# Kernel optimization log

Hardware: AMD Instinct MI355X
Metric: run time of the kernel (lower is better)

Reference implementation:

```python
import jax, jax.numpy as jnp
import numpy as np

EPS = 1e-5

def _segment_mean(src_feat, edge_index, num_targets):
    # src_feat: [Ns, D]; edge_index: [2, E] = [source_idx, target_idx]
    msgs = src_feat[edge_index[0]]                                   # [E, D] gather
    agg = jax.ops.segment_sum(msgs, edge_index[1], num_segments=num_targets)
    deg = jax.ops.segment_sum(jnp.ones((edge_index.shape[1],), src_feat.dtype),
                              edge_index[1], num_segments=num_targets)
    return agg / jnp.clip(deg, 1.0)[:, None]

def _layernorm(x, gamma, beta):
    mu = jnp.mean(x, axis=-1, keepdims=True)
    var = jnp.mean(jnp.square(x - mu), axis=-1, keepdims=True)
    return (x - mu) * jax.lax.rsqrt(var + EPS) * gamma + beta

def setup_inputs() -> dict:
    key = jax.random.key(0)
    ks = jax.random.split(key, 8)
    NU, NI, E, D = 50000, 50000, 300000, 256
    s = 1.0 / np.sqrt(D)
    return {
        "user_features": jax.random.normal(ks[0], (NU, D), jnp.float32),
        "item_features": jax.random.normal(ks[1], (NI, D), jnp.float32),
        "user_item_edge_index": jax.random.randint(ks[2], (2, E), 0, NI),
        "item_user_edge_index": jax.random.randint(ks[3], (2, E), 0, NU),
        "Wu": jax.random.uniform(ks[4], (D, D), jnp.float32, -s, s),
        "bu": jax.random.uniform(ks[5], (D,), jnp.float32, -s, s),
        "Wi": jax.random.uniform(ks[6], (D, D), jnp.float32, -s, s),
        "bi": jax.random.uniform(ks[7], (D,), jnp.float32, -s, s),
        "gamma": jnp.ones((D,), jnp.float32),
        "beta": jnp.zeros((D,), jnp.float32),
    }

def reference(user_features, item_features, user_item_edge_index, item_user_edge_index,
              Wu, bu, Wi, bi, gamma, beta):
    num_items = item_features.shape[0]
    num_users = user_features.shape[0]
    # messages into items come from users; into users come from items
    item_messages = _segment_mean(user_features, user_item_edge_index, num_items)
    user_messages = _segment_mean(item_features, item_user_edge_index, num_users)
    u_new = (user_features + user_messages) @ Wu + bu
    i_new = (item_features + item_messages) @ Wi + bi
    u_new = _layernorm(jax.nn.relu(u_new), gamma, beta)
    i_new = _layernorm(jax.nn.relu(i_new), gamma, beta)
    return (u_new, i_new)
```

## Files before the change

### kernel.cpp

```cpp
#include <hip/hip_runtime.h>
#include <hip/hip_bf16.h>

#define D 256
#define BM 64
#define BM2 32
#define LDA 264
#define LDK 72

typedef __attribute__((ext_vector_type(8))) __bf16 bf16x8;
typedef __attribute__((ext_vector_type(4))) float f32x4;

__device__ __forceinline__ float bf2f(unsigned short u) {
    union { unsigned int i; float f; } c; c.i = ((unsigned int)u) << 16; return c.f;
}
__device__ __forceinline__ float bf2f_lo(unsigned int u) {
    union { unsigned int i; float f; } c; c.i = u << 16; return c.f;
}
__device__ __forceinline__ float bf2f_hi(unsigned int u) {
    union { unsigned int i; float f; } c; c.i = u & 0xffff0000u; return c.f;
}
__device__ __forceinline__ unsigned short f2bf(float f) {
    __hip_bfloat16 h = __float2bfloat16(f);
    return *reinterpret_cast<unsigned short*>(&h);
}
__device__ __forceinline__ unsigned int pack2(float lo, float hi) {
    return (unsigned int)f2bf(lo) | ((unsigned int)f2bf(hi) << 16);
}


__global__ void k_prep(const float* __restrict__ uf, const float* __restrict__ itf,
                       const float* __restrict__ Wu, const float* __restrict__ Wi,
                       unsigned short* __restrict__ feat_bf,
                       unsigned short* __restrict__ Wt_u, unsigned short* __restrict__ Wt_i,
                       const int* __restrict__ iu_e, int Eiu,
                       const int* __restrict__ ui_e, int Eui,
                       int* __restrict__ deg, int NU,
                       size_t nfU, size_t nfTot, int nbF) {
    int b = blockIdx.x;
    if (b < nbF) {
        size_t base = ((size_t)b * 256 + threadIdx.x) * 8;
        if (base < nfTot) {
            const float* s = (base < nfU) ? (uf + base) : (itf + (base - nfU));
            float4 f0 = *(const float4*)s;
            float4 f1 = *(const float4*)(s + 4);
            ushort4 o0, o1;
            o0.x = f2bf(f0.x); o0.y = f2bf(f0.y); o0.z = f2bf(f0.z); o0.w = f2bf(f0.w);
            o1.x = f2bf(f1.x); o1.y = f2bf(f1.y); o1.z = f2bf(f1.z); o1.w = f2bf(f1.w);
            ((ushort4*)(feat_bf + base))[0] = o0;
            ((ushort4*)(feat_bf + base))[1] = o1;
        }
    } else if (b < nbF + 512) {
        int b2 = b - nbF;
        const float* W = (b2 < 256) ? Wu : Wi;
        unsigned short* Wt = (b2 < 256) ? Wt_u : Wt_i;
        int k = b2 & 255;
        int c = threadIdx.x;
        Wt[(size_t)c * 256 + k] = f2bf(W[(size_t)k * 256 + c]);
    } else {
        int e = (b - nbF - 512) * 256 + threadIdx.x;
        if (e < Eiu) {
            atomicAdd(&deg[iu_e[Eiu + e]], 1);
        } else if (e < Eiu + Eui) {
            int e2 = e - Eiu;
            atomicAdd(&deg[NU + ui_e[Eui + e2]], 1);
        }
    }
}

__global__ void k_scan_block(const int* __restrict__ deg, int N,
                             int* __restrict__ rs, int* __restrict__ bsums) {
    __shared__ int s[1024];
    int base = blockIdx.x * 1024;
    int t = threadIdx.x;
    int v = (base + t < N) ? deg[base + t] : 0;
    s[t] = v;
    __syncthreads();
    for (int off = 1; off < 1024; off <<= 1) {
        int add = (t >= off) ? s[t - off] : 0;
        __syncthreads();
        s[t] += add;
        __syncthreads();
    }
    if (base + t < N) rs[base + t + 1] = s[t];
    if (t == 1023) bsums[blockIdx.x] = s[1023];
}

__global__ void k_scan_sums(int* __restrict__ bsums, int nb) {
    __shared__ int s[1024];
    int t = threadIdx.x;
    int v = (t < nb) ? bsums[t] : 0;
    s[t] = v;
    __syncthreads();
    for (int off = 1; off < 1024; off <<= 1) {
        int add = (t >= off) ? s[t - off] : 0;
        __syncthreads();
        s[t] += add;
        __syncthreads();
    }
    if (t < nb) bsums[t] = s[t] - v;
}

__global__ void k_finalize(int N, int* __restrict__ rs, int* __restrict__ cur,
                           const int* __restrict__ bsums) {
    int i = blockIdx.x * blockDim.x + threadIdx.x;
    if (i < N) {
        int v = rs[i + 1] + bsums[i >> 10];
        rs[i + 1] = v;
        cur[i + 1] = v;
    }
    if (i == 0) { rs[0] = 0; cur[0] = 0; }
}

__global__ void k_fill2(const int* __restrict__ iu_e, int Eiu,
                        const int* __restrict__ ui_e, int Eui,
                        int* __restrict__ cur, int NU,
                        int* __restrict__ csr) {
    int e = blockIdx.x * blockDim.x + threadIdx.x;
    if (e < Eiu) {
        int d = iu_e[Eiu + e];
        int p = atomicAdd(&cur[d], 1);
        csr[p] = iu_e[e];
    } else if (e < Eiu + Eui) {
        int e2 = e - Eiu;
        int d = ui_e[Eui + e2];
        int p = atomicAdd(&cur[NU + d], 1);
        csr[p] = ui_e[e2];
    }
}

__global__ void k_msg2(const unsigned short* __restrict__ uf_bf,
                       const unsigned short* __restrict__ if_bf,
                       const int* __restrict__ rs, const int* __restrict__ csr,
                       unsigned short* __restrict__ x_u, unsigned short* __restrict__ x_i,
                       int NU, int NI) {
    int pair = (blockIdx.x * blockDim.x + threadIdx.x) >> 6;
    int lane = threadIdx.x & 63;
    int half = lane >> 5;
    int hl   = lane & 31;
    int Ntot = NU + NI;
    int wv = pair * 2 + half;
    if (wv >= Ntot) return;

    const unsigned short* src; const unsigned short* tgt; unsigned short* xo; int w;
    if (wv < NU) { src = if_bf; tgt = uf_bf; xo = x_u; w = wv; }
    else         { src = uf_bf; tgt = if_bf; xo = x_i; w = wv - NU; }

    int s0 = rs[wv], s1 = rs[wv + 1];
    float a0[8] = {}, a1[8] = {}, a2[8] = {}, a3[8] = {};

    int i = s0;
    for (; i + 4 <= s1; i += 4) {
        int e0 = csr[i], e1 = csr[i + 1], e2 = csr[i + 2], e3 = csr[i + 3];
        uint4 r0 = ((const uint4*)(src + (size_t)e0 * D))[hl];
        uint4 r1 = ((const uint4*)(src + (size_t)e1 * D))[hl];
        uint4 r2 = ((const uint4*)(src + (size_t)e2 * D))[hl];
        uint4 r3 = ((const uint4*)(src + (size_t)e3 * D))[hl];
        a0[0] += bf2f_lo(r0.x); a0[1] += bf2f_hi(r0.x); a0[2] += bf2f_lo(r0.y); a0[3] += bf2f_hi(r0.y);
        a0[4] += bf2f_lo(r0.z); a0[5] += bf2f_hi(r0.z); a0[6] += bf2f_lo(r0.w); a0[7] += bf2f_hi(r0.w);
        a1[0] += bf2f_lo(r1.x); a1[1] += bf2f_hi(r1.x); a1[2] += bf2f_lo(r1.y); a1[3] += bf2f_hi(r1.y);
        a1[4] += bf2f_lo(r1.z); a1[5] += bf2f_hi(r1.z); a1[6] += bf2f_lo(r1.w); a1[7] += bf2f_hi(r1.w);
        a2[0] += bf2f_lo(r2.x); a2[1] += bf2f_hi(r2.x); a2[2] += bf2f_lo(r2.y); a2[3] += bf2f_hi(r2.y);
        a2[4] += bf2f_lo(r2.z); a2[5] += bf2f_hi(r2.z); a2[6] += bf2f_lo(r2.w); a2[7] += bf2f_hi(r2.w);
        a3[0] += bf2f_lo(r3.x); a3[1] += bf2f_hi(r3.x); a3[2] += bf2f_lo(r3.y); a3[3] += bf2f_hi(r3.y);
        a3[4] += bf2f_lo(r3.z); a3[5] += bf2f_hi(r3.z); a3[6] += bf2f_lo(r3.w); a3[7] += bf2f_hi(r3.w);
    }
    for (; i < s1; ++i) {
        int e0 = csr[i];
        uint4 r0 = ((const uint4*)(src + (size_t)e0 * D))[hl];
        a0[0] += bf2f_lo(r0.x); a0[1] += bf2f_hi(r0.x); a0[2] += bf2f_lo(r0.y); a0[3] += bf2f_hi(r0.y);
        a0[4] += bf2f_lo(r0.z); a0[5] += bf2f_hi(r0.z); a0[6] += bf2f_lo(r0.w); a0[7] += bf2f_hi(r0.w);
    }

    int cnt = s1 - s0;
    float inv = 1.0f / (float)(cnt > 0 ? cnt : 1);
    uint4 tv = ((const uint4*)(tgt + (size_t)w * D))[hl];
    float x0 = bf2f_lo(tv.x) + (a0[0] + a1[0] + a2[0] + a3[0]) * inv;
    float x1 = bf2f_hi(tv.x) + (a0[1] + a1[1] + a2[1] + a3[1]) * inv;
    float x2 = bf2f_lo(tv.y) + (a0[2] + a1[2] + a2[2] + a3[2]) * inv;
    float x3 = bf2f_hi(tv.y) + (a0[3] + a1[3] + a2[3] + a3[3]) * inv;
    float x4 = bf2f_lo(tv.z) + (a0[4] + a1[4] + a2[4] + a3[4]) * inv;
    float x5 = bf2f_hi(tv.z) + (a0[5] + a1[5] + a2[5] + a3[5]) * inv;
    float x6 = bf2f_lo(tv.w) + (a0[6] + a1[6] + a2[6] + a3[6]) * inv;
    float x7 = bf2f_hi(tv.w) + (a0[7] + a1[7] + a2[7] + a3[7]) * inv;
    uint4 o;
    o.x = pack2(x0, x1); o.y = pack2(x2, x3); o.z = pack2(x4, x5); o.w = pack2(x6, x7);
    ((uint4*)(xo + (size_t)w * D))[hl] = o;
}

__launch_bounds__(256)
__global__ void k_gemm5(const unsigned short* __restrict__ x_u,
                        const unsigned short* __restrict__ x_i,
                        const unsigned short* __restrict__ Wt_u,
                        const unsigned short* __restrict__ Wt_i,
                        const float* __restrict__ bu, const float* __restrict__ bi,
                        const float* __restrict__ gamma, const float* __restrict__ beta,
                        int NU, int NI, int nbU, float* __restrict__ out) {
    __shared__ __align__(16) __hip_bfloat16 As[BM2][LDA];
    __shared__ float red_s[BM2][4];
    __shared__ float red_q[BM2][4];

    int b = blockIdx.x;
    bool isU = b < nbU;
    const unsigned short* X  = isU ? x_u : x_i;
    const unsigned short* Wt = isU ? Wt_u : Wt_i;
    const float* bias        = isU ? bu : bi;
    float* Y                 = isU ? out : out + (size_t)NU * D;
    int N                    = isU ? NU : NI;
    int row0 = (isU ? b : b - nbU) * BM2;

    int t = threadIdx.x;
    int lane = t & 63;
    int w = t >> 6;
    int l15 = lane & 15;
    int l4 = lane >> 4;

    {
        const uint4* Xg = (const uint4*)&X[(size_t)row0 * D];
        #pragma unroll
        for (int j = 0; j < 4; ++j) {
            int f = j * 256 + t;
            int lr = f >> 5;
            int c = f & 31;
            uint4 v = {0, 0, 0, 0};
            if (row0 + lr < N) v = Xg[(size_t)lr * 32 + c];
            *(uint4*)&As[lr][c * 8] = v;
        }
    }

    f32x4 acc[2][4];
    f32x4 zero = {0.f, 0.f, 0.f, 0.f};
    #pragma unroll
    for (int fr = 0; fr < 2; fr++)
        #pragma unroll
        for (int fc = 0; fc < 4; fc++)
            acc[fr][fc] = zero;

    __syncthreads();

    const uint4* Bg = (const uint4*)Wt;
    int colB = w * 64 + l15;
    #pragma unroll
    for (int ks8 = 0; ks8 < 8; ++ks8) {
        uint4 bq[4];
        #pragma unroll
        for (int fc = 0; fc < 4; ++fc)
            bq[fc] = Bg[(size_t)(colB + fc * 16) * 32 + ks8 * 4 + l4];
        bf16x8 af[2];
        #pragma unroll
        for (int fr = 0; fr < 2; ++fr)
            af[fr] = *(const bf16x8*)&As[fr * 16 + l15][ks8 * 32 + l4 * 8];
        #pragma unroll
        for (int fr = 0; fr < 2; ++fr)
            #pragma unroll
            for (int fc = 0; fc < 4; ++fc)
                acc[fr][fc] = __builtin_amdgcn_mfma_f32_16x16x32_bf16(
                    af[fr], *(bf16x8*)&bq[fc], acc[fr][fc], 0, 0, 0);
    }

    float bias_c[4], gam_c[4], bet_c[4];
    #pragma unroll
    for (int fc = 0; fc < 4; fc++) {
        int col = w * 64 + fc * 16 + l15;
        bias_c[fc] = bias[col];
        gam_c[fc]  = gamma[col];
        bet_c[fc]  = beta[col];
    }

    #pragma unroll
    for (int fr = 0; fr < 2; fr++) {
        #pragma unroll
        for (int r = 0; r < 4; r++) {
            int row = fr * 16 + l4 * 4 + r;
            float s = 0.f, q = 0.f;
            #pragma unroll
            for (int fc = 0; fc < 4; fc++) {
                float v = acc[fr][fc][r] + bias_c[fc];
                v = fmaxf(v, 0.f);
                acc[fr][fc][r] = v;
                s += v;
                q += v * v;
            }
            #pragma unroll
            for (int m = 1; m < 16; m <<= 1) {
                s += __shfl_xor(s, m);
                q += __shfl_xor(q, m);
            }
            if (l15 == 0) { red_s[row][w] = s; red_q[row][w] = q; }
        }
    }
    __syncthreads();

    #pragma unroll
    for (int fr = 0; fr < 2; fr++) {
        #pragma unroll
        for (int r = 0; r < 4; r++) {
            int row = fr * 16 + l4 * 4 + r;
            int grow = row0 + row;
            if (grow >= N) continue;
            float s = red_s[row][0] + red_s[row][1] + red_s[row][2] + red_s[row][3];
            float q = red_q[row][0] + red_q[row][1] + red_q[row][2] + red_q[row][3];
            float mu  = s * (1.0f / 256.0f);
            float var = q * (1.0f / 256.0f) - mu * mu;
            float rstd = rsqrtf(var + 1e-5f);
            #pragma unroll
            for (int fc = 0; fc < 4; fc++) {
                int col = w * 64 + fc * 16 + l15;
                Y[(size_t)grow * D + col] = (acc[fr][fc][r] - mu) * rstd * gam_c[fc] + bet_c[fc];
            }
        }
    }
}


__global__ void k_hist(const int* __restrict__ dst, int E, int* __restrict__ deg) {
    int e = blockIdx.x * blockDim.x + threadIdx.x;
    if (e < E) atomicAdd(&deg[dst[e]], 1);
}

__global__ void k_finalize_rs(int N, int* __restrict__ rs, const int* __restrict__ bsums) {
    int i = blockIdx.x * blockDim.x + threadIdx.x;
    if (i < N) rs[i + 1] += bsums[i >> 10];
    if (i == 0) rs[0] = 0;
}

__global__ void k_fill(const int* __restrict__ src, const int* __restrict__ dst, int E,
                       const int* __restrict__ rs, int* __restrict__ cursor,
                       int* __restrict__ csr) {
    int e = blockIdx.x * blockDim.x + threadIdx.x;
    if (e < E) {
        int d = dst[e];
        int p = atomicAdd(&cursor[d], 1);
        csr[rs[d] + p] = src[e];
    }
}

__global__ void k_msg_x(const float* __restrict__ srcf, const float* __restrict__ tgtf,
                        const int* __restrict__ rs, const int* __restrict__ csr,
                        int N, float* __restrict__ xout) {
    int wave = (blockIdx.x * blockDim.x + threadIdx.x) >> 6;
    int lane = threadIdx.x & 63;
    if (wave >= N) return;
    int s0 = rs[wave], s1 = rs[wave + 1];
    float4 acc = make_float4(0.f, 0.f, 0.f, 0.f);
    for (int i = s0; i < s1; i++) {
        int s = csr[i];
        float4 f = *(const float4*)&srcf[(size_t)s * D + lane * 4];
        acc.x += f.x; acc.y += f.y; acc.z += f.z; acc.w += f.w;
    }
    int cnt = s1 - s0;
    float inv = 1.0f / (float)(cnt > 0 ? cnt : 1);
    float4 t = *(const float4*)&tgtf[(size_t)wave * D + lane * 4];
    float4 x;
    x.x = t.x + acc.x * inv;
    x.y = t.y + acc.y * inv;
    x.z = t.z + acc.z * inv;
    x.w = t.w + acc.w * inv;
    *(float4*)&xout[(size_t)wave * D + lane * 4] = x;
}

__global__ void k_wcvt(const float* __restrict__ W0, const float* __restrict__ W1,
                       __hip_bfloat16* __restrict__ Wt0, __hip_bfloat16* __restrict__ Wt1) {
    int b = blockIdx.x;
    const float* W = (b < 256) ? W0 : W1;
    __hip_bfloat16* Wt = (b < 256) ? Wt0 : Wt1;
    int k = b & 255;
    int c = threadIdx.x;
    Wt[(size_t)c * 256 + k] = __float2bfloat16(W[(size_t)k * 256 + c]);
}

__launch_bounds__(256)
__global__ void k_gemm_mfma_ln(const float* __restrict__ X,
                               const __hip_bfloat16* __restrict__ Wt,
                               const float* __restrict__ bias,
                               const float* __restrict__ gamma,
                               const float* __restrict__ beta,
                               int N, float* __restrict__ Y) {
    __shared__ __hip_bfloat16 As[BM][LDK];
    __shared__ __hip_bfloat16 Bs[D][LDK];
    __shared__ float red_s[BM][4];
    __shared__ float red_q[BM][4];

    int t = threadIdx.x;
    int lane = t & 63;
    int w = t >> 6;
    int l15 = lane & 15;
    int l4 = lane >> 4;
    int row0 = blockIdx.x * BM;

    f32x4 acc[4][4];
    f32x4 zero = {0.f, 0.f, 0.f, 0.f};
    #pragma unroll
    for (int fr = 0; fr < 4; fr++)
        #pragma unroll
        for (int fc = 0; fc < 4; fc++)
            acc[fr][fc] = zero;

    for (int k0 = 0; k0 < D; k0 += 64) {
        {
            int i = t >> 2;
            int kq = (t & 3) * 16;
            int r = row0 + i;
            float4 f[4];
            if (r < N) {
                const float4* p = (const float4*)&X[(size_t)r * D + k0 + kq];
                f[0] = p[0]; f[1] = p[1]; f[2] = p[2]; f[3] = p[3];
            } else {
                float4 z4 = make_float4(0.f, 0.f, 0.f, 0.f);
                f[0] = z4; f[1] = z4; f[2] = z4; f[3] = z4;
            }
            __hip_bfloat16 vb[16];
            #pragma unroll
            for (int q = 0; q < 4; q++) {
                vb[q * 4 + 0] = __float2bfloat16(f[q].x);
                vb[q * 4 + 1] = __float2bfloat16(f[q].y);
                vb[q * 4 + 2] = __float2bfloat16(f[q].z);
                vb[q * 4 + 3] = __float2bfloat16(f[q].w);
            }
            *(uint4*)&As[i][kq]     = *(uint4*)&vb[0];
            *(uint4*)&As[i][kq + 8] = *(uint4*)&vb[8];
        }
        #pragma unroll
        for (int pass = 0; pass < 4; pass++) {
            int c = pass * 64 + (t >> 2);
            int kq = (t & 3) * 16;
            const uint4* p = (const uint4*)&Wt[(size_t)c * D + k0 + kq];
            uint4 b0 = p[0], b1 = p[1];
            *(uint4*)&Bs[c][kq]     = b0;
            *(uint4*)&Bs[c][kq + 8] = b1;
        }
        __syncthreads();

        #pragma unroll
        for (int ks = 0; ks < 2; ks++) {
            bf16x8 af[4], bg[4];
            #pragma unroll
            for (int fr = 0; fr < 4; fr++)
                af[fr] = *(const bf16x8*)&As[fr * 16 + l15][ks * 32 + l4 * 8];
            #pragma unroll
            for (int fc = 0; fc < 4; fc++)
                bg[fc] = *(const bf16x8*)&Bs[w * 64 + fc * 16 + l15][ks * 32 + l4 * 8];
            #pragma unroll
            for (int fr = 0; fr < 4; fr++)
                #pragma unroll
                for (int fc = 0; fc < 4; fc++)
                    acc[fr][fc] = __builtin_amdgcn_mfma_f32_16x16x32_bf16(
                        af[fr], bg[fc], acc[fr][fc], 0, 0, 0);
        }
        __syncthreads();
    }

    float bias_c[4], gam_c[4], bet_c[4];
    #pragma unroll
    for (int fc = 0; fc < 4; fc++) {
        int col = w * 64 + fc * 16 + l15;
        bias_c[fc] = bias[col];
        gam_c[fc]  = gamma[col];
        bet_c[fc]  = beta[col];
    }

    #pragma unroll
    for (int fr = 0; fr < 4; fr++) {
        #pragma unroll
        for (int r = 0; r < 4; r++) {
            int row = fr * 16 + l4 * 4 + r;
            float s = 0.f, q = 0.f;
            #pragma unroll
            for (int fc = 0; fc < 4; fc++) {
                float v = acc[fr][fc][r] + bias_c[fc];
                v = fmaxf(v, 0.f);
                acc[fr][fc][r] = v;
                s += v;
                q += v * v;
            }
            #pragma unroll
            for (int m = 1; m < 16; m <<= 1) {
                s += __shfl_xor(s, m);
                q += __shfl_xor(q, m);
            }
            if (l15 == 0) { red_s[row][w] = s; red_q[row][w] = q; }
        }
    }
    __syncthreads();

    #pragma unroll
    for (int fr = 0; fr < 4; fr++) {
        #pragma unroll
        for (int r = 0; r < 4; r++) {
            int row = fr * 16 + l4 * 4 + r;
            int grow = row0 + row;
            if (grow >= N) continue;
            float s = red_s[row][0] + red_s[row][1] + red_s[row][2] + red_s[row][3];
            float q = red_q[row][0] + red_q[row][1] + red_q[row][2] + red_q[row][3];
            float mu  = s * (1.0f / 256.0f);
            float var = q * (1.0f / 256.0f) - mu * mu;
            float rstd = rsqrtf(var + 1e-5f);
            #pragma unroll
            for (int fc = 0; fc < 4; fc++) {
                int col = w * 64 + fc * 16 + l15;
                Y[(size_t)grow * D + col] = (acc[fr][fc][r] - mu) * rstd * gam_c[fc] + bet_c[fc];
            }
        }
    }
}


extern "C" void kernel_launch(void* const* d_in, const int* in_sizes, int n_in,
                              void* d_out, int out_size, void* d_ws, size_t ws_size,
                              hipStream_t stream) {
    const float* uf    = (const float*)d_in[0];
    const float* itf   = (const float*)d_in[1];
    const int*   ui_e  = (const int*)d_in[2];
    const int*   iu_e  = (const int*)d_in[3];
    const float* Wu    = (const float*)d_in[4];
    const float* bu    = (const float*)d_in[5];
    const float* Wi    = (const float*)d_in[6];
    const float* bi    = (const float*)d_in[7];
    const float* gamma = (const float*)d_in[8];
    const float* beta  = (const float*)d_in[9];

    int NU  = in_sizes[0] / D;
    int NI  = in_sizes[1] / D;
    int Eui = in_sizes[2] / 2;
    int Eiu = in_sizes[3] / 2;
    int Nmax = NU > NI ? NU : NI;
    int Ntot = NU + NI;
    int Etot = Eiu + Eui;

    float* out   = (float*)d_out;
    size_t nfU = (size_t)NU * D;
    size_t nfI = (size_t)NI * D;
    size_t nfTot = nfU + nfI;

    unsigned short* uf_bf = (unsigned short*)d_ws;
    unsigned short* if_bf = uf_bf + nfU;
    unsigned short* x_u   = if_bf + nfI;
    unsigned short* x_i   = x_u + nfU;
    unsigned short* Wt_u2 = x_i + nfI;
    unsigned short* Wt_i2 = Wt_u2 + 65536;
    int* deg2  = (int*)(Wt_i2 + 65536);
    int* rs2   = deg2 + Ntot;
    int* cur2  = rs2 + Ntot + 1;
    int* bsums = cur2 + Ntot + 1;
    int* csr2  = bsums + 1024;
    size_t needed = (size_t)((char*)(csr2 + Etot) - (char*)d_ws);

    if (ws_size >= needed) {
        int nbF = (int)((nfTot + 2047) / 2048);
        int nbH = (Etot + 255) / 256;
        hipMemsetAsync(deg2, 0, (size_t)Ntot * sizeof(int), stream);
        k_prep<<<nbF + 512 + nbH, 256, 0, stream>>>(uf, itf, Wu, Wi, uf_bf, Wt_u2, Wt_i2,
                                                    iu_e, Eiu, ui_e, Eui, deg2, NU,
                                                    nfU, nfTot, nbF);
        int nb = (Ntot + 1023) / 1024;
        k_scan_block<<<nb, 1024, 0, stream>>>(deg2, Ntot, rs2, bsums);
        k_scan_sums<<<1, 1024, 0, stream>>>(bsums, nb);
        k_finalize<<<(Ntot + 255) / 256, 256, 0, stream>>>(Ntot, rs2, cur2, bsums);
        k_fill2<<<nbH, 256, 0, stream>>>(iu_e, Eiu, ui_e, Eui, cur2, NU, csr2);
        int pairs = (Ntot + 1) / 2;
        k_msg2<<<(pairs + 3) / 4, 256, 0, stream>>>(uf_bf, if_bf, rs2, csr2, x_u, x_i, NU, NI);
        int nbU = (NU + BM2 - 1) / BM2;
        int nbI = (NI + BM2 - 1) / BM2;
        k_gemm5<<<nbU + nbI, 256, 0, stream>>>(x_u, x_i, Wt_u2, Wt_i2, bu, bi, gamma, beta,
                                               NU, NI, nbU, out);
        return;
    }

    float* u_out = out;
    float* i_out = out + nfU;
    __hip_bfloat16* Wt_u = (__hip_bfloat16*)d_ws;
    __hip_bfloat16* Wt_i = Wt_u + 256 * 256;
    int* deg    = (int*)(Wt_i + 256 * 256);
    int* rs     = deg + Nmax;
    int* bs     = rs + Nmax + 1;
    int* cursor = bs + 1024;
    int* csr    = cursor + Nmax;

    k_wcvt<<<512, 256, 0, stream>>>(Wu, Wi, Wt_u, Wt_i);

    auto run_side = [&](const float* srcf, const float* tgtf, const int* edges, int E,
                        int N, const __hip_bfloat16* Wt, const float* bias, float* y) {
        const int* esrc = edges;
        const int* edst = edges + E;
        hipMemsetAsync(deg, 0, (size_t)N * sizeof(int), stream);
        hipMemsetAsync(cursor, 0, (size_t)N * sizeof(int), stream);
        k_hist<<<(E + 255) / 256, 256, 0, stream>>>(edst, E, deg);
        int nb = (N + 1023) / 1024;
        k_scan_block<<<nb, 1024, 0, stream>>>(deg, N, rs, bs);
        k_scan_sums<<<1, 1024, 0, stream>>>(bs, nb);
        k_finalize_rs<<<(N + 255) / 256, 256, 0, stream>>>(N, rs, bs);
        k_fill<<<(E + 255) / 256, 256, 0, stream>>>(esrc, edst, E, rs, cursor, csr);
        k_msg_x<<<(N + 3) / 4, 256, 0, stream>>>(srcf, tgtf, rs, csr, N, y);
        k_gemm_mfma_ln<<<(N + BM - 1) / BM, 256, 0, stream>>>(y, Wt, bias, gamma, beta, N, y);
    };

    run_side(itf, uf, iu_e, Eiu, NU, Wt_u, bu, u_out);
    run_side(uf, itf, ui_e, Eui, NI, Wt_i, bi, i_out);
}
```

Before: 218.0 us.

## Overlap item message aggregation with user GEMM in a mixed kernel

```diff
diff --git a/kernel.cpp b/kernel.cpp
--- a/kernel.cpp
+++ b/kernel.cpp
@@ -25,6 +25,163 @@
 }
 __device__ __forceinline__ unsigned int pack2(float lo, float hi) {
     return (unsigned int)f2bf(lo) | ((unsigned int)f2bf(hi) << 16);
+}
+
+
+__device__ __forceinline__ void msg_pair_body(
+    const unsigned short* __restrict__ src, const unsigned short* __restrict__ tgt,
+    const int* __restrict__ rs, const int* __restrict__ csr,
+    unsigned short* __restrict__ xo, int rsBase, int N, int pair, int lane) {
+    int half = lane >> 5;
+    int hl   = lane & 31;
+    int w = pair * 2 + half;
+    if (w >= N) return;
+    int wv = rsBase + w;
+    int s0 = rs[wv], s1 = rs[wv + 1];
+    float a0[8] = {}, a1[8] = {}, a2[8] = {}, a3[8] = {};
+    int i = s0;
+    for (; i + 4 <= s1; i += 4) {
+        int e0 = csr[i], e1 = csr[i + 1], e2 = csr[i + 2], e3 = csr[i + 3];
+        uint4 r0 = ((const uint4*)(src + (size_t)e0 * D))[hl];
+        uint4 r1 = ((const uint4*)(src + (size_t)e1 * D))[hl];
+        uint4 r2 = ((const uint4*)(src + (size_t)e2 * D))[hl];
+        uint4 r3 = ((const uint4*)(src + (size_t)e3 * D))[hl];
+        a0[0] += bf2f_lo(r0.x); a0[1] += bf2f_hi(r0.x); a0[2] += bf2f_lo(r0.y); a0[3] += bf2f_hi(r0.y);
+        a0[4] += bf2f_lo(r0.z); a0[5] += bf2f_hi(r0.z); a0[6] += bf2f_lo(r0.w); a0[7] += bf2f_hi(r0.w);
+        a1[0] += bf2f_lo(r1.x); a1[1] += bf2f_hi(r1.x); a1[2] += bf2f_lo(r1.y); a1[3] += bf2f_hi(r1.y);
+        a1[4] += bf2f_lo(r1.z); a1[5] += bf2f_hi(r1.z); a1[6] += bf2f_lo(r1.w); a1[7] += bf2f_hi(r1.w);
+        a2[0] += bf2f_lo(r2.x); a2[1] += bf2f_hi(r2.x); a2[2] += bf2f_lo(r2.y); a2[3] += bf2f_hi(r2.y);
+        a2[4] += bf2f_lo(r2.z); a2[5] += bf2f_hi(r2.z); a2[6] += bf2f_lo(r2.w); a2[7] += bf2f_hi(r2.w);
+        a3[0] += bf2f_lo(r3.x); a3[1] += bf2f_hi(r3.x); a3[2] += bf2f_lo(r3.y); a3[3] += bf2f_hi(r3.y);
+        a3[4] += bf2f_lo(r3.z); a3[5] += bf2f_hi(r3.z); a3[6] += bf2f_lo(r3.w); a3[7] += bf2f_hi(r3.w);
+    }
+    for (; i < s1; ++i) {
+        int e0 = csr[i];
+        uint4 r0 = ((const uint4*)(src + (size_t)e0 * D))[hl];
+        a0[0] += bf2f_lo(r0.x); a0[1] += bf2f_hi(r0.x); a0[2] += bf2f_lo(r0.y); a0[3] += bf2f_hi(r0.y);
+        a0[4] += bf2f_lo(r0.z); a0[5] += bf2f_hi(r0.z); a0[6] += bf2f_lo(r0.w); a0[7] += bf2f_hi(r0.w);
+    }
+    int cnt = s1 - s0;
+    float inv = 1.0f / (float)(cnt > 0 ? cnt : 1);
+    uint4 tv = ((const uint4*)(tgt + (size_t)w * D))[hl];
+    float x0 = bf2f_lo(tv.x) + (a0[0] + a1[0] + a2[0] + a3[0]) * inv;
+    float x1 = bf2f_hi(tv.x) + (a0[1] + a1[1] + a2[1] + a3[1]) * inv;
+    float x2 = bf2f_lo(tv.y) + (a0[2] + a1[2] + a2[2] + a3[2]) * inv;
+    float x3 = bf2f_hi(tv.y) + (a0[3] + a1[3] + a2[3] + a3[3]) * inv;
+    float x4 = bf2f_lo(tv.z) + (a0[4] + a1[4] + a2[4] + a3[4]) * inv;
+    float x5 = bf2f_hi(tv.z) + (a0[5] + a1[5] + a2[5] + a3[5]) * inv;
+    float x6 = bf2f_lo(tv.w) + (a0[6] + a1[6] + a2[6] + a3[6]) * inv;
+    float x7 = bf2f_hi(tv.w) + (a0[7] + a1[7] + a2[7] + a3[7]) * inv;
+    uint4 o;
+    o.x = pack2(x0, x1); o.y = pack2(x2, x3); o.z = pack2(x4, x5); o.w = pack2(x6, x7);
+    ((uint4*)(xo + (size_t)w * D))[hl] = o;
+}
+
+__device__ __forceinline__ void gemm_tile_body(
+    const unsigned short* __restrict__ X, const unsigned short* __restrict__ Wt,
+    const float* __restrict__ bias, const float* __restrict__ gamma,
+    const float* __restrict__ beta, int N, float* __restrict__ Y, int row0, int t,
+    __hip_bfloat16 (*As)[LDA], float (*red_s)[4], float (*red_q)[4]) {
+    int lane = t & 63;
+    int w = t >> 6;
+    int l15 = lane & 15;
+    int l4 = lane >> 4;
+
+    {
+        const uint4* Xg = (const uint4*)&X[(size_t)row0 * D];
+        #pragma unroll
+        for (int j = 0; j < 4; ++j) {
+            int f = j * 256 + t;
+            int lr = f >> 5;
+            int c = f & 31;
+            uint4 v = {0, 0, 0, 0};
+            if (row0 + lr < N) v = Xg[(size_t)lr * 32 + c];
+            *(uint4*)&As[lr][c * 8] = v;
+        }
+    }
+
+    f32x4 acc[2][4];
+    f32x4 zero = {0.f, 0.f, 0.f, 0.f};
+    #pragma unroll
+    for (int fr = 0; fr < 2; fr++)
+        #pragma unroll
+        for (int fc = 0; fc < 4; fc++)
+            acc[fr][fc] = zero;
+
+    __syncthreads();
+
+    const uint4* Bg = (const uint4*)Wt;
+    int colB = w * 64 + l15;
+    #pragma unroll
+    for (int ks8 = 0; ks8 < 8; ++ks8) {
+        uint4 bq[4];
+        #pragma unroll
+        for (int fc = 0; fc < 4; ++fc)
+            bq[fc] = Bg[(size_t)(colB + fc * 16) * 32 + ks8 * 4 + l4];
+        bf16x8 af[2];
+        #pragma unroll
+        for (int fr = 0; fr < 2; ++fr)
+            af[fr] = *(const bf16x8*)&As[fr * 16 + l15][ks8 * 32 + l4 * 8];
+        #pragma unroll
+        for (int fr = 0; fr < 2; ++fr)
+            #pragma unroll
+            for (int fc = 0; fc < 4; ++fc)
+                acc[fr][fc] = __builtin_amdgcn_mfma_f32_16x16x32_bf16(
+                    af[fr], *(bf16x8*)&bq[fc], acc[fr][fc], 0, 0, 0);
+    }
+
+    float bias_c[4], gam_c[4], bet_c[4];
+    #pragma unroll
+    for (int fc = 0; fc < 4; fc++) {
+        int col = w * 64 + fc * 16 + l15;
+        bias_c[fc] = bias[col];
+        gam_c[fc]  = gamma[col];
+        bet_c[fc]  = beta[col];
+    }
+
+    #pragma unroll
+    for (int fr = 0; fr < 2; fr++) {
+        #pragma unroll
+        for (int r = 0; r < 4; r++) {
+            int row = fr * 16 + l4 * 4 + r;
+            float s = 0.f, q = 0.f;
+            #pragma unroll
+            for (int fc = 0; fc < 4; fc++) {
+                float v = acc[fr][fc][r] + bias_c[fc];
+                v = fmaxf(v, 0.f);
+                acc[fr][fc][r] = v;
+                s += v;
+                q += v * v;
+            }
+            #pragma unroll
+            for (int m = 1; m < 16; m <<= 1) {
+                s += __shfl_xor(s, m);
+                q += __shfl_xor(q, m);
+            }
+            if (l15 == 0) { red_s[row][w] = s; red_q[row][w] = q; }
+        }
+    }
+    __syncthreads();
+
+    #pragma unroll
+    for (int fr = 0; fr < 2; fr++) {
+        #pragma unroll
+        for (int r = 0; r < 4; r++) {
+            int row = fr * 16 + l4 * 4 + r;
+            int grow = row0 + row;
+            if (grow >= N) continue;
+            float s = red_s[row][0] + red_s[row][1] + red_s[row][2] + red_s[row][3];
+            float q = red_q[row][0] + red_q[row][1] + red_q[row][2] + red_q[row][3];
+            float mu  = s * (1.0f / 256.0f);
+            float var = q * (1.0f / 256.0f) - mu * mu;
+            float rstd = rsqrtf(var + 1e-5f);
+            #pragma unroll
+            for (int fc = 0; fc < 4; fc++) {
+                int col = w * 64 + fc * 16 + l15;
+                Y[(size_t)grow * D + col] = (acc[fr][fc][r] - mu) * rstd * gam_c[fc] + bet_c[fc];
+            }
+        }
+    }
 }
 
 
@@ -128,187 +285,48 @@
     }
 }
 
-__global__ void k_msg2(const unsigned short* __restrict__ uf_bf,
+__global__ void k_msgU(const unsigned short* __restrict__ uf_bf,
                        const unsigned short* __restrict__ if_bf,
                        const int* __restrict__ rs, const int* __restrict__ csr,
-                       unsigned short* __restrict__ x_u, unsigned short* __restrict__ x_i,
-                       int NU, int NI) {
+                       unsigned short* __restrict__ x_u, int NU) {
     int pair = (blockIdx.x * blockDim.x + threadIdx.x) >> 6;
-    int lane = threadIdx.x & 63;
-    int half = lane >> 5;
-    int hl   = lane & 31;
-    int Ntot = NU + NI;
-    int wv = pair * 2 + half;
-    if (wv >= Ntot) return;
-
-    const unsigned short* src; const unsigned short* tgt; unsigned short* xo; int w;
-    if (wv < NU) { src = if_bf; tgt = uf_bf; xo = x_u; w = wv; }
-    else         { src = uf_bf; tgt = if_bf; xo = x_i; w = wv - NU; }
-
-    int s0 = rs[wv], s1 = rs[wv + 1];
-    float a0[8] = {}, a1[8] = {}, a2[8] = {}, a3[8] = {};
-
-    int i = s0;
-    for (; i + 4 <= s1; i += 4) {
-        int e0 = csr[i], e1 = csr[i + 1], e2 = csr[i + 2], e3 = csr[i + 3];
-        uint4 r0 = ((const uint4*)(src + (size_t)e0 * D))[hl];
-        uint4 r1 = ((const uint4*)(src + (size_t)e1 * D))[hl];
-        uint4 r2 = ((const uint4*)(src + (size_t)e2 * D))[hl];
-        uint4 r3 = ((const uint4*)(src + (size_t)e3 * D))[hl];
-        a0[0] += bf2f_lo(r0.x); a0[1] += bf2f_hi(r0.x); a0[2] += bf2f_lo(r0.y); a0[3] += bf2f_hi(r0.y);
-        a0[4] += bf2f_lo(r0.z); a0[5] += bf2f_hi(r0.z); a0[6] += bf2f_lo(r0.w); a0[7] += bf2f_hi(r0.w);
-        a1[0] += bf2f_lo(r1.x); a1[1] += bf2f_hi(r1.x); a1[2] += bf2f_lo(r1.y); a1[3] += bf2f_hi(r1.y);
-        a1[4] += bf2f_lo(r1.z); a1[5] += bf2f_hi(r1.z); a1[6] += bf2f_lo(r1.w); a1[7] += bf2f_hi(r1.w);
-        a2[0] += bf2f_lo(r2.x); a2[1] += bf2f_hi(r2.x); a2[2] += bf2f_lo(r2.y); a2[3] += bf2f_hi(r2.y);
-        a2[4] += bf2f_lo(r2.z); a2[5] += bf2f_hi(r2.z); a2[6] += bf2f_lo(r2.w); a2[7] += bf2f_hi(r2.w);
-        a3[0] += bf2f_lo(r3.x); a3[1] += bf2f_hi(r3.x); a3[2] += bf2f_lo(r3.y); a3[3] += bf2f_hi(r3.y);
-        a3[4] += bf2f_lo(r3.z); a3[5] += bf2f_hi(r3.z); a3[6] += bf2f_lo(r3.w); a3[7] += bf2f_hi(r3.w);
-    }
-    for (; i < s1; ++i) {
-        int e0 = csr[i];
-        uint4 r0 = ((const uint4*)(src + (size_t)e0 * D))[hl];
-        a0[0] += bf2f_lo(r0.x); a0[1] += bf2f_hi(r0.x); a0[2] += bf2f_lo(r0.y); a0[3] += bf2f_hi(r0.y);
-        a0[4] += bf2f_lo(r0.z); a0[5] += bf2f_hi(r0.z); a0[6] += bf2f_lo(r0.w); a0[7] += bf2f_hi(r0.w);
-    }
-
-    int cnt = s1 - s0;
-    float inv = 1.0f / (float)(cnt > 0 ? cnt : 1);
-    uint4 tv = ((const uint4*)(tgt + (size_t)w * D))[hl];
-    float x0 = bf2f_lo(tv.x) + (a0[0] + a1[0] + a2[0] + a3[0]) * inv;
-    float x1 = bf2f_hi(tv.x) + (a0[1] + a1[1] + a2[1] + a3[1]) * inv;
-    float x2 = bf2f_lo(tv.y) + (a0[2] + a1[2] + a2[2] + a3[2]) * inv;
-    float x3 = bf2f_hi(tv.y) + (a0[3] + a1[3] + a2[3] + a3[3]) * inv;
-    float x4 = bf2f_lo(tv.z) + (a0[4] + a1[4] + a2[4] + a3[4]) * inv;
-    float x5 = bf2f_hi(tv.z) + (a0[5] + a1[5] + a2[5] + a3[5]) * inv;
-    float x6 = bf2f_lo(tv.w) + (a0[6] + a1[6] + a2[6] + a3[6]) * inv;
-    float x7 = bf2f_hi(tv.w) + (a0[7] + a1[7] + a2[7] + a3[7]) * inv;
-    uint4 o;
-    o.x = pack2(x0, x1); o.y = pack2(x2, x3); o.z = pack2(x4, x5); o.w = pack2(x6, x7);
-    ((uint4*)(xo + (size_t)w * D))[hl] = o;
+    msg_pair_body(if_bf, uf_bf, rs, csr, x_u, 0, NU, pair, threadIdx.x & 63);
 }
 
 __launch_bounds__(256)
-__global__ void k_gemm5(const unsigned short* __restrict__ x_u,
-                        const unsigned short* __restrict__ x_i,
-                        const unsigned short* __restrict__ Wt_u,
-                        const unsigned short* __restrict__ Wt_i,
-                        const float* __restrict__ bu, const float* __restrict__ bi,
-                        const float* __restrict__ gamma, const float* __restrict__ beta,
-                        int NU, int NI, int nbU, float* __restrict__ out) {
+__global__ void k_mix(const unsigned short* __restrict__ uf_bf,
+                      const unsigned short* __restrict__ if_bf,
+                      const int* __restrict__ rs, const int* __restrict__ csr,
+                      unsigned short* __restrict__ x_i,
+                      const unsigned short* __restrict__ x_u,
+                      const unsigned short* __restrict__ Wt_u,
+                      const float* __restrict__ bu,
+                      const float* __restrict__ gamma, const float* __restrict__ beta,
+                      int NU, int NI, int nbMsgI, float* __restrict__ out) {
     __shared__ __align__(16) __hip_bfloat16 As[BM2][LDA];
     __shared__ float red_s[BM2][4];
     __shared__ float red_q[BM2][4];
-
-    int b = blockIdx.x;
-    bool isU = b < nbU;
-    const unsigned short* X  = isU ? x_u : x_i;
-    const unsigned short* Wt = isU ? Wt_u : Wt_i;
-    const float* bias        = isU ? bu : bi;
-    float* Y                 = isU ? out : out + (size_t)NU * D;
-    int N                    = isU ? NU : NI;
-    int row0 = (isU ? b : b - nbU) * BM2;
-
     int t = threadIdx.x;
-    int lane = t & 63;
-    int w = t >> 6;
-    int l15 = lane & 15;
-    int l4 = lane >> 4;
-
-    {
-        const uint4* Xg = (const uint4*)&X[(size_t)row0 * D];
-        #pragma unroll
-        for (int j = 0; j < 4; ++j) {
-            int f = j * 256 + t;
-            int lr = f >> 5;
-            int c = f & 31;
-            uint4 v = {0, 0, 0, 0};
-            if (row0 + lr < N) v = Xg[(size_t)lr * 32 + c];
-            *(uint4*)&As[lr][c * 8] = v;
-        }
-    }
-
-    f32x4 acc[2][4];
-    f32x4 zero = {0.f, 0.f, 0.f, 0.f};
-    #pragma unroll
-    for (int fr = 0; fr < 2; fr++)
-        #pragma unroll
-        for (int fc = 0; fc < 4; fc++)
-            acc[fr][fc] = zero;
-
-    __syncthreads();
-
-    const uint4* Bg = (const uint4*)Wt;
-    int colB = w * 64 + l15;
-    #pragma unroll
-    for (int ks8 = 0; ks8 < 8; ++ks8) {
-        uint4 bq[4];
-        #pragma unroll
-        for (int fc = 0; fc < 4; ++fc)
-            bq[fc] = Bg[(size_t)(colB + fc * 16) * 32 + ks8 * 4 + l4];
-        bf16x8 af[2];
-        #pragma unroll
-        for (int fr = 0; fr < 2; ++fr)
-            af[fr] = *(const bf16x8*)&As[fr * 16 + l15][ks8 * 32 + l4 * 8];
-        #pragma unroll
-        for (int fr = 0; fr < 2; ++fr)
-            #pragma unroll
-            for (int fc = 0; fc < 4; ++fc)
-                acc[fr][fc] = __builtin_amdgcn_mfma_f32_16x16x32_bf16(
-                    af[fr], *(bf16x8*)&bq[fc], acc[fr][fc], 0, 0, 0);
-    }
-
-    float bias_c[4], gam_c[4], bet_c[4];
-    #pragma unroll
-    for (int fc = 0; fc < 4; fc++) {
-        int col = w * 64 + fc * 16 + l15;
-        bias_c[fc] = bias[col];
-        gam_c[fc]  = gamma[col];
-        bet_c[fc]  = beta[col];
-    }
-
-    #pragma unroll
-    for (int fr = 0; fr < 2; fr++) {
-        #pragma unroll
-        for (int r = 0; r < 4; r++) {
-            int row = fr * 16 + l4 * 4 + r;
-            float s = 0.f, q = 0.f;
-            #pragma unroll
-            for (int fc = 0; fc < 4; fc++) {
-                float v = acc[fr][fc][r] + bias_c[fc];
-                v = fmaxf(v, 0.f);
-                acc[fr][fc][r] = v;
-                s += v;
-                q += v * v;
-            }
-            #pragma unroll
-            for (int m = 1; m < 16; m <<= 1) {
-                s += __shfl_xor(s, m);
-                q += __shfl_xor(q, m);
-            }
-            if (l15 == 0) { red_s[row][w] = s; red_q[row][w] = q; }
-        }
-    }
-    __syncthreads();
-
-    #pragma unroll
-    for (int fr = 0; fr < 2; fr++) {
-        #pragma unroll
-        for (int r = 0; r < 4; r++) {
-            int row = fr * 16 + l4 * 4 + r;
-            int grow = row0 + row;
-            if (grow >= N) continue;
-            float s = red_s[row][0] + red_s[row][1] + red_s[row][2] + red_s[row][3];
-            float q = red_q[row][0] + red_q[row][1] + red_q[row][2] + red_q[row][3];
-            float mu  = s * (1.0f / 256.0f);
-            float var = q * (1.0f / 256.0f) - mu * mu;
-            float rstd = rsqrtf(var + 1e-5f);
-            #pragma unroll
-            for (int fc = 0; fc < 4; fc++) {
-                int col = w * 64 + fc * 16 + l15;
-                Y[(size_t)grow * D + col] = (acc[fr][fc][r] - mu) * rstd * gam_c[fc] + bet_c[fc];
-            }
-        }
-    }
+    if (blockIdx.x < nbMsgI) {
+        int pair = (blockIdx.x * 256 + t) >> 6;
+        msg_pair_body(uf_bf, if_bf, rs, csr, x_i, NU, NI, pair, t & 63);
+    } else {
+        int b = blockIdx.x - nbMsgI;
+        gemm_tile_body(x_u, Wt_u, bu, gamma, beta, NU, out, b * BM2, t, As, red_s, red_q);
+    }
+}
+
+__launch_bounds__(256)
+__global__ void k_gemmI(const unsigned short* __restrict__ x_i,
+                        const unsigned short* __restrict__ Wt_i,
+                        const float* __restrict__ bi,
+                        const float* __restrict__ gamma, const float* __restrict__ beta,
+                        int NU, int NI, float* __restrict__ out) {
+    __shared__ __align__(16) __hip_bfloat16 As[BM2][LDA];
+    __shared__ float red_s[BM2][4];
+    __shared__ float red_q[BM2][4];
+    gemm_tile_body(x_i, Wt_i, bi, gamma, beta, NI, out + (size_t)NU * D,
+                   blockIdx.x * BM2, threadIdx.x, As, red_s, red_q);
 }
 
 
@@ -556,12 +574,17 @@
         k_scan_sums<<<1, 1024, 0, stream>>>(bsums, nb);
         k_finalize<<<(Ntot + 255) / 256, 256, 0, stream>>>(Ntot, rs2, cur2, bsums);
         k_fill2<<<nbH, 256, 0, stream>>>(iu_e, Eiu, ui_e, Eui, cur2, NU, csr2);
-        int pairs = (Ntot + 1) / 2;
-        k_msg2<<<(pairs + 3) / 4, 256, 0, stream>>>(uf_bf, if_bf, rs2, csr2, x_u, x_i, NU, NI);
-        int nbU = (NU + BM2 - 1) / BM2;
-        int nbI = (NI + BM2 - 1) / BM2;
-        k_gemm5<<<nbU + nbI, 256, 0, stream>>>(x_u, x_i, Wt_u2, Wt_i2, bu, bi, gamma, beta,
-                                               NU, NI, nbU, out);
+
+        int pairsU = (NU + 1) / 2;
+        k_msgU<<<(pairsU + 3) / 4, 256, 0, stream>>>(uf_bf, if_bf, rs2, csr2, x_u, NU);
+        int pairsI = (NI + 1) / 2;
+        int nbMsgI = (pairsI + 3) / 4;
+        int nbGemmU = (NU + BM2 - 1) / BM2;
+        k_mix<<<nbMsgI + nbGemmU, 256, 0, stream>>>(uf_bf, if_bf, rs2, csr2, x_i, x_u,
+                                                    Wt_u2, bu, gamma, beta,
+                                                    NU, NI, nbMsgI, out);
+        int nbGemmI = (NI + BM2 - 1) / BM2;
+        k_gemmI<<<nbGemmI, 256, 0, stream>>>(x_i, Wt_i2, bi, gamma, beta, NU, NI, out);
         return;
     }
 
```

After: 238.5 us. 1.09x slower.

## Make GEMM+LayerNorm kernel persistent with weights staged once in LDS

Applied to the files above, without the earlier changes.

```diff
diff --git a/kernel.cpp b/kernel.cpp
--- a/kernel.cpp
+++ b/kernel.cpp
@@ -5,6 +5,7 @@
 #define BM 64
 #define BM2 32
 #define LDA 264
+#define LDB 258
 #define LDK 72
 
 typedef __attribute__((ext_vector_type(8))) __bf16 bf16x8;
@@ -187,26 +188,28 @@
     ((uint4*)(xo + (size_t)w * D))[hl] = o;
 }
 
-__launch_bounds__(256)
-__global__ void k_gemm5(const unsigned short* __restrict__ x_u,
+__launch_bounds__(512)
+__global__ void k_gemm7(const unsigned short* __restrict__ x_u,
                         const unsigned short* __restrict__ x_i,
                         const unsigned short* __restrict__ Wt_u,
                         const unsigned short* __restrict__ Wt_i,
                         const float* __restrict__ bu, const float* __restrict__ bi,
                         const float* __restrict__ gamma, const float* __restrict__ beta,
-                        int NU, int NI, int nbU, float* __restrict__ out) {
+                        int NU, int NI, float* __restrict__ out) {
+    __shared__ __align__(16) __hip_bfloat16 Bs[256][LDB];
     __shared__ __align__(16) __hip_bfloat16 As[BM2][LDA];
-    __shared__ float red_s[BM2][4];
-    __shared__ float red_q[BM2][4];
+    __shared__ float red_s[BM2][8];
+    __shared__ float red_q[BM2][8];
 
     int b = blockIdx.x;
-    bool isU = b < nbU;
+    bool isU = b < 256;
     const unsigned short* X  = isU ? x_u : x_i;
     const unsigned short* Wt = isU ? Wt_u : Wt_i;
     const float* bias        = isU ? bu : bi;
     float* Y                 = isU ? out : out + (size_t)NU * D;
     int N                    = isU ? NU : NI;
-    int row0 = (isU ? b : b - nbU) * BM2;
+    int idx0 = b & 255;
+    int ntiles = (N + BM2 - 1) / BM2;
 
     int t = threadIdx.x;
     int lane = t & 63;
@@ -215,99 +218,120 @@
     int l4 = lane >> 4;
 
     {
-        const uint4* Xg = (const uint4*)&X[(size_t)row0 * D];
-        #pragma unroll
-        for (int j = 0; j < 4; ++j) {
-            int f = j * 256 + t;
-            int lr = f >> 5;
+        const uint4* Wg = (const uint4*)Wt;
+        #pragma unroll
+        for (int j = 0; j < 16; ++j) {
+            int f = j * 512 + t;
+            int col = f >> 5;
             int c = f & 31;
-            uint4 v = {0, 0, 0, 0};
-            if (row0 + lr < N) v = Xg[(size_t)lr * 32 + c];
-            *(uint4*)&As[lr][c * 8] = v;
-        }
-    }
-
-    f32x4 acc[2][4];
-    f32x4 zero = {0.f, 0.f, 0.f, 0.f};
+            uint4 v = Wg[(size_t)col * 32 + c];
+            *(uint4*)&Bs[col][c * 8] = v;
+        }
+    }
+
+    float bias_c[2], gam_c[2], bet_c[2];
     #pragma unroll
-    for (int fr = 0; fr < 2; fr++)
-        #pragma unroll
-        for (int fc = 0; fc < 4; fc++)
-            acc[fr][fc] = zero;
-
-    __syncthreads();
-
-    const uint4* Bg = (const uint4*)Wt;
-    int colB = w * 64 + l15;
-    #pragma unroll
-    for (int ks8 = 0; ks8 < 8; ++ks8) {
-        uint4 bq[4];
-        #pragma unroll
-        for (int fc = 0; fc < 4; ++fc)
-            bq[fc] = Bg[(size_t)(colB + fc * 16) * 32 + ks8 * 4 + l4];
-        bf16x8 af[2];
-        #pragma unroll
-        for (int fr = 0; fr < 2; ++fr)
-            af[fr] = *(const bf16x8*)&As[fr * 16 + l15][ks8 * 32 + l4 * 8];
-        #pragma unroll
-        for (int fr = 0; fr < 2; ++fr)
-            #pragma unroll
-            for (int fc = 0; fc < 4; ++fc)
-                acc[fr][fc] = __builtin_amdgcn_mfma_f32_16x16x32_bf16(
-                    af[fr], *(bf16x8*)&bq[fc], acc[fr][fc], 0, 0, 0);
-    }
-
-    float bias_c[4], gam_c[4], bet_c[4];
-    #pragma unroll
-    for (int fc = 0; fc < 4; fc++) {
-        int col = w * 64 + fc * 16 + l15;
+    for (int fc = 0; fc < 2; ++fc) {
+        int col = w * 32 + fc * 16 + l15;
         bias_c[fc] = bias[col];
         gam_c[fc]  = gamma[col];
         bet_c[fc]  = beta[col];
     }
 
-    #pragma unroll
-    for (int fr = 0; fr < 2; fr++) {
-        #pragma unroll
-        for (int r = 0; r < 4; r++) {
-            int row = fr * 16 + l4 * 4 + r;
-            float s = 0.f, q = 0.f;
-            #pragma unroll
-            for (int fc = 0; fc < 4; fc++) {
-                float v = acc[fr][fc][r] + bias_c[fc];
-                v = fmaxf(v, 0.f);
-                acc[fr][fc][r] = v;
-                s += v;
-                q += v * v;
+    int f0 = t, f1 = 512 + t;
+    int lr0 = f0 >> 5, c0 = f0 & 31;
+    int lr1 = f1 >> 5, c1 = f1 & 31;
+
+    int tile = idx0;
+    uint4 aR0 = {0, 0, 0, 0}, aR1 = {0, 0, 0, 0};
+    if (tile < ntiles) {
+        const uint4* Xg = (const uint4*)&X[(size_t)tile * BM2 * D];
+        if (tile * BM2 + lr0 < N) aR0 = Xg[(size_t)lr0 * 32 + c0];
+        if (tile * BM2 + lr1 < N) aR1 = Xg[(size_t)lr1 * 32 + c1];
+    }
+    __syncthreads();
+
+    for (; tile < ntiles; tile += 256) {
+        int row0 = tile * BM2;
+        *(uint4*)&As[lr0][c0 * 8] = aR0;
+        *(uint4*)&As[lr1][c1 * 8] = aR1;
+        __syncthreads();
+
+        int nt = tile + 256;
+        if (nt < ntiles) {
+            const uint4* Xg = (const uint4*)&X[(size_t)nt * BM2 * D];
+            uint4 z = {0, 0, 0, 0};
+            aR0 = z; aR1 = z;
+            if (nt * BM2 + lr0 < N) aR0 = Xg[(size_t)lr0 * 32 + c0];
+            if (nt * BM2 + lr1 < N) aR1 = Xg[(size_t)lr1 * 32 + c1];
+        }
+
+        f32x4 acc[2][2];
+        f32x4 zero = {0.f, 0.f, 0.f, 0.f};
+        acc[0][0] = zero; acc[0][1] = zero; acc[1][0] = zero; acc[1][1] = zero;
+        #pragma unroll
+        for (int ks8 = 0; ks8 < 8; ++ks8) {
+            bf16x8 af[2], bg[2];
+            #pragma unroll
+            for (int fr = 0; fr < 2; ++fr)
+                af[fr] = *(const bf16x8*)&As[fr * 16 + l15][ks8 * 32 + l4 * 8];
+            #pragma unroll
+            for (int fc = 0; fc < 2; ++fc)
+                bg[fc] = *(const bf16x8*)&Bs[w * 32 + fc * 16 + l15][ks8 * 32 + l4 * 8];
+            #pragma unroll
+            for (int fr = 0; fr < 2; ++fr)
+                #pragma unroll
+                for (int fc = 0; fc < 2; ++fc)
+                    acc[fr][fc] = __builtin_amdgcn_mfma_f32_16x16x32_bf16(
+                        af[fr], bg[fc], acc[fr][fc], 0, 0, 0);
+        }
+
+        #pragma unroll
+        for (int fr = 0; fr < 2; ++fr) {
+            #pragma unroll
+            for (int r = 0; r < 4; ++r) {
+                int row = fr * 16 + l4 * 4 + r;
+                float s = 0.f, q = 0.f;
+                #pragma unroll
+                for (int fc = 0; fc < 2; ++fc) {
+                    float v = acc[fr][fc][r] + bias_c[fc];
+                    v = fmaxf(v, 0.f);
+                    acc[fr][fc][r] = v;
+                    s += v;
+                    q += v * v;
+                }
+                #pragma unroll
+                for (int m = 1; m < 16; m <<= 1) {
+                    s += __shfl_xor(s, m);
+                    q += __shfl_xor(q, m);
+                }
+                if (l15 == 0) { red_s[row][w] = s; red_q[row][w] = q; }
             }
-            #pragma unroll
-            for (int m = 1; m < 16; m <<= 1) {
-                s += __shfl_xor(s, m);
-                q += __shfl_xor(q, m);
+        }
+        __syncthreads();
+
+        #pragma unroll
+        for (int fr = 0; fr < 2; ++fr) {
+            #pragma unroll
+            for (int r = 0; r < 4; ++r) {
+                int row = fr * 16 + l4 * 4 + r;
+                int grow = row0 + row;
+                if (grow >= N) continue;
+                float s = red_s[row][0] + red_s[row][1] + red_s[row][2] + red_s[row][3]
+                        + red_s[row][4] + red_s[row][5] + red_s[row][6] + red_s[row][7];
+                float q = red_q[row][0] + red_q[row][1] + red_q[row][2] + red_q[row][3]
+                        + red_q[row][4] + red_q[row][5] + red_q[row][6] + red_q[row][7];
+                float mu  = s * (1.0f / 256.0f);
+                float var = q * (1.0f / 256.0f) - mu * mu;
+                float rstd = rsqrtf(var + 1e-5f);
+                #pragma unroll
+                for (int fc = 0; fc < 2; ++fc) {
+                    int col = w * 32 + fc * 16 + l15;
+                    Y[(size_t)grow * D + col] = (acc[fr][fc][r] - mu) * rstd * gam_c[fc] + bet_c[fc];
+                }
             }
-            if (l15 == 0) { red_s[row][w] = s; red_q[row][w] = q; }
-        }
-    }
-    __syncthreads();
-
-    #pragma unroll
-    for (int fr = 0; fr < 2; fr++) {
-        #pragma unroll
-        for (int r = 0; r < 4; r++) {
-            int row = fr * 16 + l4 * 4 + r;
-            int grow = row0 + row;
-            if (grow >= N) continue;
-            float s = red_s[row][0] + red_s[row][1] + red_s[row][2] + red_s[row][3];
-            float q = red_q[row][0] + red_q[row][1] + red_q[row][2] + red_q[row][3];
-            float mu  = s * (1.0f / 256.0f);
-            float var = q * (1.0f / 256.0f) - mu * mu;
-            float rstd = rsqrtf(var + 1e-5f);
-            #pragma unroll
-            for (int fc = 0; fc < 4; fc++) {
-                int col = w * 64 + fc * 16 + l15;
-                Y[(size_t)grow * D + col] = (acc[fr][fc][r] - mu) * rstd * gam_c[fc] + bet_c[fc];
-            }
-        }
+        }
+        __syncthreads();
     }
 }
 
@@ -558,10 +582,8 @@
         k_fill2<<<nbH, 256, 0, stream>>>(iu_e, Eiu, ui_e, Eui, cur2, NU, csr2);
         int pairs = (Ntot + 1) / 2;
         k_msg2<<<(pairs + 3) / 4, 256, 0, stream>>>(uf_bf, if_bf, rs2, csr2, x_u, x_i, NU, NI);
-        int nbU = (NU + BM2 - 1) / BM2;
-        int nbI = (NI + BM2 - 1) / BM2;
-        k_gemm5<<<nbU + nbI, 256, 0, stream>>>(x_u, x_i, Wt_u2, Wt_i2, bu, bi, gamma, beta,
-                                               NU, NI, nbU, out);
+        k_gemm7<<<512, 512, 0, stream>>>(x_u, x_i, Wt_u2, Wt_i2, bu, bi, gamma, beta,
+                                         NU, NI, out);
         return;
     }
 
```

Measured after the change: 225.2 us. 1.03x slower.
